# Kernel optimization log

Measured on AMD Instinct MI355X. Metric: run time of the kernel, lower is better.

Reference implementation:

```python
import jax, jax.numpy as jnp
import numpy as np

B, T, H, W = 4, 32, 160, 320
NF, FPF = 8, 8          # num_filters, features_per_filter
SPEED_DIM = 8           # speed_embedding output width
U = 64                  # internal LTC neurons (wiring units)
S = NF * FPF + SPEED_DIM  # 72 sensory inputs
M = 1                   # motor (output) neurons
ODE_UNFOLDS = 6
EPS = 1e-8


def setup_inputs() -> dict:
    key = jax.random.key(0)
    k = jax.random.split(key, 20)
    f32 = jnp.float32
    sp = (H // 8) * (W // 8)  # spatial size per filter after 3 stride-2 convs = 800
    d = {}
    d["input_sequence"] = jax.random.normal(k[0], (B, T, 3, H, W), f32)
    d["speed_sequence"] = jax.random.uniform(k[1], (B, T, 1), f32)
    # conv head params
    d["conv1_w"] = jax.random.normal(k[2], (16, 3, 5, 5), f32) * 0.05
    d["conv1_b"] = jnp.zeros((16,), f32)
    d["conv2_w"] = jax.random.normal(k[3], (32, 16, 5, 5), f32) * 0.05
    d["conv2_b"] = jnp.zeros((32,), f32)
    d["conv3_w"] = jax.random.normal(k[4], (NF, 32, 5, 5), f32) * 0.05
    d["conv3_b"] = jnp.zeros((NF,), f32)
    d["head_w"] = jax.random.normal(k[5], (NF, sp, FPF), f32) * 0.02  # per-filter Linear
    d["head_b"] = jnp.zeros((NF, FPF), f32)
    # speed embedding MLP (Dropout is identity at inference)
    d["se_w1"] = jax.random.normal(k[6], (1, 16), f32) * 0.5
    d["se_b1"] = jnp.zeros((16,), f32)
    d["se_w2"] = jax.random.normal(k[7], (16, SPEED_DIM), f32) * 0.3
    d["se_b2"] = jnp.zeros((SPEED_DIM,), f32)
    # LTC cell params (ncps-style init ranges)
    d["input_w"] = jnp.ones((S,), f32)
    d["input_b"] = jnp.zeros((S,), f32)
    d["gleak"] = jax.random.uniform(k[8], (U,), f32, 0.001, 1.0)
    d["vleak"] = jax.random.uniform(k[9], (U,), f32, -0.2, 0.2)
    d["cm"] = jax.random.uniform(k[10], (U,), f32, 0.4, 0.6)
    d["sigma"] = jax.random.uniform(k[11], (U, U), f32, 3.0, 8.0)
    d["mu"] = jax.random.uniform(k[12], (U, U), f32, 0.3, 0.8)
    d["w_syn"] = jax.random.uniform(k[13], (U, U), f32, 0.001, 1.0)
    d["erev"] = jnp.asarray(jax.random.bernoulli(k[14], 0.5, (U, U)), f32) * 2.0 - 1.0
    d["sensory_sigma"] = jax.random.uniform(k[15], (S, U), f32, 3.0, 8.0)
    d["sensory_mu"] = jax.random.uniform(k[16], (S, U), f32, 0.3, 0.8)
    d["sensory_w"] = jax.random.uniform(k[17], (S, U), f32, 0.001, 1.0)
    d["sensory_erev"] = jnp.asarray(jax.random.bernoulli(k[18], 0.5, (S, U)), f32) * 2.0 - 1.0
    d["output_w"] = jnp.ones((M,), f32)
    d["output_b"] = jnp.zeros((M,), f32)
    return d


def _conv(x, w, b, stride):
    y = jax.lax.conv_general_dilated(
        x, w, (stride, stride), [(2, 2), (2, 2)],
        dimension_numbers=("NCHW", "OIHW", "NCHW"))
    return jax.nn.relu(y + b[None, :, None, None])


def reference(input_sequence, speed_sequence, conv1_w, conv1_b, conv2_w, conv2_b,
              conv3_w, conv3_b, head_w, head_b, se_w1, se_b1, se_w2, se_b2,
              input_w, input_b, gleak, vleak, cm, sigma, mu, w_syn, erev,
              sensory_sigma, sensory_mu, sensory_w, sensory_erev, output_w, output_b):
    Bv, Tv = input_sequence.shape[:2]
    # ---- conv head over all frames at once ----
    x = input_sequence.reshape(Bv * Tv, 3, H, W)
    x = _conv(x, conv1_w, conv1_b, 2)
    x = _conv(x, conv2_w, conv2_b, 2)
    x = _conv(x, conv3_w, conv3_b, 2)          # [N, NF, H/8, W/8]
    x = x.reshape(Bv * Tv, NF, -1)             # [N, NF, 800]
    feats = jnp.einsum("nfp,fpk->nfk", x, head_w) + head_b  # per-filter Linear
    feats = feats.reshape(Bv, Tv, NF * FPF)    # [B, T, 64]
    # global-std normalization (torch .std() uses ddof=1)
    feats = feats / (jnp.std(feats, ddof=1) + 1e-5)
    # ---- speed embedding (vectorized over B,T) ----
    s = speed_sequence[..., :1]                # [B, T, 1]
    emb = jnp.tanh(jax.nn.relu(s @ se_w1 + se_b1) @ se_w2 + se_b2)  # [B, T, 8]
    xs = jnp.concatenate([feats, emb], axis=-1)   # [B, T, S]
    xs = jnp.swapaxes(xs, 0, 1)                   # [T, B, S]
    cm_t = cm * ODE_UNFOLDS  # cm / (elapsed_time / ode_unfolds), elapsed_time = 1.0

    def step(v, x_t):
        inp = x_t * input_w + input_b  # affine input mapping, [B, S]
        s_act = sensory_w * jax.nn.sigmoid((inp[:, :, None] - sensory_mu) * sensory_sigma)  # [B,S,U]
        w_num_s = jnp.sum(s_act * sensory_erev, axis=1)
        w_den_s = jnp.sum(s_act, axis=1)
        for _ in range(ODE_UNFOLDS):  # semi-implicit Euler unfolds
            w_act = w_syn * jax.nn.sigmoid((v[:, :, None] - mu) * sigma)  # [B,U,U]
            w_num = jnp.sum(w_act * erev, axis=1) + w_num_s
            w_den = jnp.sum(w_act, axis=1) + w_den_s
            v = (cm_t * v + gleak * vleak + w_num) / (cm_t + gleak + w_den + EPS)
        out = v[:, :M] * output_w + output_b  # affine output mapping on motor neurons
        return v, (out, v)

    v0 = jnp.zeros((Bv, U), feats.dtype)
    v_last, (outs, hs) = jax.lax.scan(step, v0, xs)
    readout = jnp.swapaxes(outs, 0, 1)  # [B, T, M]
    all_h = jnp.swapaxes(hs, 0, 1)      # [B, T, U]
    return readout, v_last, all_h
```

## Files before the change

### kernel.cpp

```cpp
#include <hip/hip_runtime.h>
#include <math.h>

#define BB 4
#define TT 32
#define NF 8
#define FPF 8
#define SDIM 8
#define UU 64
#define SS 72
#define UNFOLDS 6

typedef short short8 __attribute__((ext_vector_type(8)));
typedef float f32x4 __attribute__((ext_vector_type(4)));
union Frag { uint4 u; short8 s; };

__device__ __forceinline__ float fast_sigmoid(float x) {
    float e = exp2f(-1.44269504f * x);
    return __builtin_amdgcn_rcpf(1.0f + e);
}

__device__ __forceinline__ ushort f2b(float f) {
    union { float f; uint u; } a;
    a.f = f;
    uint u = a.u;
    return (ushort)((u + 0x7FFFu + ((u >> 16) & 1u)) >> 16);
}

__device__ __forceinline__ float bcast_lane(float v, int lane) {
    return __uint_as_float(__builtin_amdgcn_readlane(__float_as_uint(v), lane));
}

__device__ __forceinline__ void cvt_body(const float* __restrict__ in,
                                         ushort* __restrict__ outp, int idx) {
    int x = idx % 320;
    int r = idx / 320;
    int y = r % 160;
    int n = r / 160;
    const float* base = in + ((size_t)n * 3 * 160 + y) * 320 + x;
    float c0 = base[0];
    float c1 = base[160 * 320];
    float c2 = base[2 * 160 * 320];
    uint2 pk;
    pk.x = (uint)f2b(c0) | ((uint)f2b(c1) << 16);
    pk.y = (uint)f2b(c2);
    *(uint2*)(outp + ((size_t)((n * 164 + y + 2) * 328) + (x + 2)) * 4) = pk;
}

template <int HP, int WP, int H, int W, int CH>
__device__ __forceinline__ void halo_body(ushort* __restrict__ buf, int bid) {
    constexpr int TOPBOT = 2 * WP;
    constexpr int SIDE = WP - W;
    constexpr int NH = 2 * TOPBOT + H * SIDE;
    int idx = bid * 256 + threadIdx.x;
    if (idx >= 128 * NH) return;
    int n = idx / NH;
    int h = idx - n * NH;
    int y, x;
    if (h < TOPBOT) {
        y = h / WP;
        x = h % WP;
    } else if (h < 2 * TOPBOT) {
        int hh = h - TOPBOT;
        y = H + 2 + hh / WP;
        x = hh % WP;
    } else {
        int hh = h - 2 * TOPBOT;
        y = 2 + hh / SIDE;
        int xi = hh % SIDE;
        x = (xi < 2) ? xi : (W + xi);
    }
    ushort* p = buf + (((size_t)n * HP + y) * WP + x) * CH;
    if constexpr (CH == 4) {
        *(uint2*)p = make_uint2(0u, 0u);
    } else {
        uint4 z = make_uint4(0u, 0u, 0u, 0u);
#pragma unroll
        for (int i = 0; i < CH / 8; i++) *(uint4*)(p + i * 8) = z;
    }
}

__device__ __forceinline__ uint4 pack8(const ushort v[8]) {
    uint4 u;
    u.x = (uint)v[0] | ((uint)v[1] << 16);
    u.y = (uint)v[2] | ((uint)v[3] << 16);
    u.z = (uint)v[4] | ((uint)v[5] << 16);
    u.w = (uint)v[6] | ((uint)v[7] << 16);
    return u;
}

__device__ __forceinline__ void wswz1_body(const float* __restrict__ w, uint4* __restrict__ o,
                                           int i) {
    int lane = i & 63, s = i >> 6;
    int oc = lane & 15, q = lane >> 4;
    ushort v[8];
#pragma unroll
    for (int j = 0; j < 8; j++) {
        int k = q * 8 + j;
        int kx = k >> 2, c = k & 3;
        float f = (kx < 5 && c < 3) ? w[((oc * 3 + c) * 5 + s) * 5 + kx] : 0.f;
        v[j] = f2b(f);
    }
    o[i] = pack8(v);
}
__device__ __forceinline__ void wswz2_body(const float* __restrict__ w, uint4* __restrict__ o,
                                           int i) {
    int lane = i & 63;
    int ct = (i >> 6) & 1;
    int s = i >> 7;
    int ky = s / 3, kxp = s % 3;
    int oc = ct * 16 + (lane & 15);
    int q = lane >> 4, h = q >> 1;
    int kx = 2 * kxp + h;
    ushort v[8];
#pragma unroll
    for (int j = 0; j < 8; j++) {
        int ch = (q & 1) * 8 + j;
        float f = (kx < 5) ? w[((oc * 16 + ch) * 5 + ky) * 5 + kx] : 0.f;
        v[j] = f2b(f);
    }
    o[i] = pack8(v);
}
__device__ __forceinline__ void wswz3_body(const float* __restrict__ w, uint4* __restrict__ o,
                                           int i) {
    int lane = i & 63, s = i >> 6;
    int ky = s / 5, kx = s % 5;
    int oc = lane & 15, q = lane >> 4;
    ushort v[8];
#pragma unroll
    for (int j = 0; j < 8; j++) {
        int ch = q * 8 + j;
        float f = (oc < 8) ? w[((oc * 32 + ch) * 5 + ky) * 5 + kx] : 0.f;
        v[j] = f2b(f);
    }
    o[i] = pack8(v);
}

__global__ __launch_bounds__(256) void prep_kernel(
    const float* __restrict__ in_seq, ushort* __restrict__ inp1, ushort* __restrict__ c1out,
    ushort* __restrict__ c2out, const float* __restrict__ c1w, const float* __restrict__ c2w,
    const float* __restrict__ c3w, uint4* __restrict__ wz1, uint4* __restrict__ wz2,
    uint4* __restrict__ wz3) {
    int bid = blockIdx.x;
    if (bid < 25600) {
        cvt_body(in_seq, inp1, bid * 256 + threadIdx.x);
    } else if (bid < 25600 + 2032) {
        int hb = bid - 25600;
        if (hb < 1296)
            halo_body<164, 328, 160, 320, 4>(inp1, hb);
        else if (hb < 1296 + 488)
            halo_body<84, 164, 80, 160, 16>(c1out, hb - 1296);
        else
            halo_body<44, 84, 40, 80, 32>(c2out, hb - 1784);
    } else {
        int i = (bid - 27632) * 256 + threadIdx.x;
        if (i < 320)
            wswz1_body(c1w, wz1, i);
        else if (i < 2240)
            wswz2_body(c2w, wz2, i - 320);
        else
            wswz3_body(c3w, wz3, i - 2240);
    }
}

__global__ __launch_bounds__(256) void conv1_mfma(const ushort* __restrict__ inp,
                                                  const uint4* __restrict__ wswz,
                                                  const float* __restrict__ bias,
                                                  ushort* __restrict__ outp) {
    const int lane = threadIdx.x & 63;
    const int wid = threadIdx.x >> 6;
    const int col = lane & 15, q = lane >> 4;

    Frag A[5];
#pragma unroll
    for (int s = 0; s < 5; s++) A[s].u = wswz[s * 64 + lane];
    float b0 = bias[q * 4 + 0], b1 = bias[q * 4 + 1], b2 = bias[q * 4 + 2], b3 = bias[q * 4 + 3];

    int gw = blockIdx.x * 4 + wid;
#pragma unroll
    for (int t = 0; t < 4; t++) {
        int p0 = gw * 64 + t * 16;
        int n = p0 / 12800;
        int rem = p0 - n * 12800;
        int oy = rem / 160;
        int ox0 = rem - oy * 160;
        int ox = ox0 + col;
        uint e0 = ((uint)(n * 164 + oy * 2) * 328u + (uint)(ox * 2 + 2 * q)) * 4u;
        f32x4 acc = {0.f, 0.f, 0.f, 0.f};
#pragma unroll
        for (int s = 0; s < 5; s++) {
            Frag B;
            B.u = *(const uint4*)(inp + e0 + (uint)s * (328u * 4u));
            acc = __builtin_amdgcn_mfma_f32_16x16x32_bf16(A[s].s, B.s, acc, 0, 0, 0);
        }
        uint oe = ((uint)(n * 84 + oy + 2) * 164u + (uint)(ox + 2)) * 16u + q * 4u;
        uint2 pk;
        pk.x = (uint)f2b(fmaxf(acc[0] + b0, 0.f)) | ((uint)f2b(fmaxf(acc[1] + b1, 0.f)) << 16);
        pk.y = (uint)f2b(fmaxf(acc[2] + b2, 0.f)) | ((uint)f2b(fmaxf(acc[3] + b3, 0.f)) << 16);
        *(uint2*)(outp + oe) = pk;
    }
}

__global__ __launch_bounds__(256) void conv2_mfma(const ushort* __restrict__ inp,
                                                  const uint4* __restrict__ wswz,
                                                  const float* __restrict__ bias,
                                                  ushort* __restrict__ outp) {
    const int lane = threadIdx.x & 63;
    const int wid = threadIdx.x >> 6;
    const int col = lane & 15, q = lane >> 4;
    const int h = q >> 1, chh = q & 1;

    int gw = blockIdx.x * 4 + wid;
    uint eb[4];
#pragma unroll
    for (int t = 0; t < 4; t++) {
        int p0 = gw * 64 + t * 16;
        int n = p0 / 3200;
        int rem = p0 - n * 3200;
        int oy = rem / 80;
        int ox0 = rem - oy * 80;
        eb[t] = ((uint)(n * 84 + oy * 2) * 164u + (uint)((ox0 + col) * 2 + h)) * 16u + chh * 8u;
    }
    f32x4 acc[4][2];
#pragma unroll
    for (int t = 0; t < 4; t++) {
        acc[t][0] = {0.f, 0.f, 0.f, 0.f};
        acc[t][1] = {0.f, 0.f, 0.f, 0.f};
    }
#pragma unroll
    for (int s = 0; s < 15; s++) {
        const int ky = s / 3, kxp = s % 3;
        Frag A0, A1;
        A0.u = wswz[(s * 2 + 0) * 64 + lane];
        A1.u = wswz[(s * 2 + 1) * 64 + lane];
        const uint d = (uint)ky * (164u * 16u) + (uint)kxp * 32u;
#pragma unroll
        for (int t = 0; t < 4; t++) {
            Frag B;
            B.u = *(const uint4*)(inp + eb[t] + d);
            acc[t][0] = __builtin_amdgcn_mfma_f32_16x16x32_bf16(A0.s, B.s, acc[t][0], 0, 0, 0);
            acc[t][1] = __builtin_amdgcn_mfma_f32_16x16x32_bf16(A1.s, B.s, acc[t][1], 0, 0, 0);
        }
    }
    float ba[2][4];
#pragma unroll
    for (int c = 0; c < 2; c++)
#pragma unroll
        for (int r = 0; r < 4; r++) ba[c][r] = bias[c * 16 + q * 4 + r];
#pragma unroll
    for (int t = 0; t < 4; t++) {
        int p0 = gw * 64 + t * 16;
        int n = p0 / 3200;
        int rem = p0 - n * 3200;
        int oy = rem / 80;
        int ox0 = rem - oy * 80;
        int ox = ox0 + col;
        uint oe = ((uint)(n * 44 + oy + 2) * 84u + (uint)(ox + 2)) * 32u;
#pragma unroll
        for (int c = 0; c < 2; c++) {
            uint2 pk;
            pk.x = (uint)f2b(fmaxf(acc[t][c][0] + ba[c][0], 0.f)) |
                   ((uint)f2b(fmaxf(acc[t][c][1] + ba[c][1], 0.f)) << 16);
            pk.y = (uint)f2b(fmaxf(acc[t][c][2] + ba[c][2], 0.f)) |
                   ((uint)f2b(fmaxf(acc[t][c][3] + ba[c][3], 0.f)) << 16);
            *(uint2*)(outp + oe + (uint)c * 16u + (uint)q * 4u) = pk;
        }
    }
}

__global__ __launch_bounds__(256) void conv3_mfma(const ushort* __restrict__ inp,
                                                  const uint4* __restrict__ wswz,
                                                  const float* __restrict__ bias,
                                                  float* __restrict__ outp) {
    const int lane = threadIdx.x & 63;
    const int wid = threadIdx.x >> 6;
    const int col = lane & 15, q = lane >> 4;

    int gw = blockIdx.x * 4 + wid;
    uint eb[4];
#pragma unroll
    for (int t = 0; t < 4; t++) {
        int p0 = gw * 64 + t * 16;
        int n = p0 / 800;
        int pix = p0 - n * 800 + col;
        int oy = pix / 40;
        int ox = pix - oy * 40;
        eb[t] = ((uint)(n * 44 + oy * 2) * 84u + (uint)(ox * 2)) * 32u + q * 8u;
    }
    f32x4 acc[4];
#pragma unroll
    for (int t = 0; t < 4; t++) acc[t] = {0.f, 0.f, 0.f, 0.f};
#pragma unroll
    for (int s = 0; s < 25; s++) {
        const int ky = s / 5, kx = s % 5;
        Frag A;
        A.u = wswz[s * 64 + lane];
        const uint d = ((uint)ky * 84u + (uint)kx) * 32u;
#pragma unroll
        for (int t = 0; t < 4; t++) {
            Frag B;
            B.u = *(const uint4*)(inp + eb[t] + d);
            acc[t] = __builtin_amdgcn_mfma_f32_16x16x32_bf16(A.s, B.s, acc[t], 0, 0, 0);
        }
    }
    if (q < 2) {
        float b0 = bias[q * 4 + 0], b1 = bias[q * 4 + 1];
        float b2 = bias[q * 4 + 2], b3 = bias[q * 4 + 3];
#pragma unroll
        for (int t = 0; t < 4; t++) {
            int p0 = gw * 64 + t * 16;
            int n = p0 / 800;
            int p = p0 - n * 800 + col;
            float4 v;
            v.x = fmaxf(acc[t][0] + b0, 0.f);
            v.y = fmaxf(acc[t][1] + b1, 0.f);
            v.z = fmaxf(acc[t][2] + b2, 0.f);
            v.w = fmaxf(acc[t][3] + b3, 0.f);
            *(float4*)(outp + ((size_t)n * 800 + p) * 8 + q * 4) = v;
        }
    }
}

__global__ __launch_bounds__(256) void head_kernel(const float* __restrict__ x,
                                                   const float* __restrict__ hw,
                                                   const float* __restrict__ hb,
                                                   float* __restrict__ feats) {
    __shared__ float part[4][64];
    int n = blockIdx.x;
    int tid = threadIdx.x;
    int lane = tid & 63;
    int c = tid >> 6;
    int f = lane >> 3;
    int k = lane & 7;
    const float* xb = x + (size_t)n * 800 * 8 + f;
    const float* wb = hw + ((size_t)f * 800) * FPF + k;
    float acc = 0.0f;
    for (int p = c * 200; p < c * 200 + 200; p++)
        acc = fmaf(xb[(size_t)p * 8], wb[(size_t)p * FPF], acc);
    part[c][lane] = acc;
    __syncthreads();
    if (c == 0)
        feats[n * 64 + lane] = part[0][lane] + part[1][lane] + part[2][lane] + part[3][lane] +
                               hb[lane];
}

__global__ __launch_bounds__(256) void sensory256(
    const float* __restrict__ feats, const float* __restrict__ speed,
    const float* __restrict__ sew1, const float* __restrict__ seb1,
    const float* __restrict__ sew2, const float* __restrict__ seb2,
    const float* __restrict__ inw, const float* __restrict__ inb,
    const float* __restrict__ ssig, const float* __restrict__ smu,
    const float* __restrict__ sw, const float* __restrict__ serev,
    float* __restrict__ wns, float* __restrict__ wds) {
    __shared__ float2 red[256];
    __shared__ float2 part[4][64];
    int bid = blockIdx.x;
    int t = bid >> 2;
    int b = bid & 3;
    int tid = threadIdx.x;
    int u = tid & 63;
    int c = tid >> 6;
    int n = b * TT + t;

    float s = 0.0f, q = 0.0f;
    for (int i = tid; i < 8192; i += 256) {
        float x = feats[i];
        s += x;
        q += x * x;
    }
    red[tid] = make_float2(s, q);
    __syncthreads();
    for (int off = 128; off > 0; off >>= 1) {
        if (tid < off) {
            float2 o = red[tid + off];
            float2 m = red[tid];
            red[tid] = make_float2(m.x + o.x, m.y + o.y);
        }
        __syncthreads();
    }
    float mean = red[0].x / 8192.0f;
    float var = fmaxf((red[0].y - 8192.0f * mean * mean) / 8191.0f, 0.0f);
    float inv = 1.0f / (sqrtf(var) + 1e-5f);

    float sp = speed[n];
    float hh[16];
#pragma unroll
    for (int j = 0; j < 16; j++) hh[j] = fmaxf(fmaf(sp, sew1[j], seb1[j]), 0.0f);
    float embv[SDIM];
#pragma unroll
    for (int k = 0; k < SDIM; k++) {
        float a = seb2[k];
#pragma unroll
        for (int j = 0; j < 16; j++) a = fmaf(hh[j], sew2[j * SDIM + k], a);
        embv[k] = tanhf(a);
    }

    float num = 0.0f, den = 0.0f;
    int ss0 = c * 18;
#pragma unroll
    for (int i = 0; i < 18; i++) {
        int ss = ss0 + i;
        float xsv = (ss < 64) ? feats[n * 64 + ss] * inv : embv[ss - 64];
        float inp = fmaf(xsv, inw[ss], inb[ss]);
        int idx = ss * UU + u;
        float x = (inp - smu[idx]) * ssig[idx];
        float act = sw[idx] * fast_sigmoid(x);
        num = fmaf(act, serev[idx], num);
        den += act;
    }
    part[c][u] = make_float2(num, den);
    __syncthreads();
    if (c == 0) {
        float2 p0 = part[0][u], p1 = part[1][u], p2 = part[2][u], p3 = part[3][u];
        wns[bid * UU + u] = p0.x + p1.x + p2.x + p3.x;
        wds[bid * UU + u] = p0.y + p1.y + p2.y + p3.y;
    }
}

__global__ __launch_bounds__(512, 1) void scan_kernel(
    const float* __restrict__ wns, const float* __restrict__ wds,
    const float* __restrict__ gleak, const float* __restrict__ vleak,
    const float* __restrict__ cm, const float* __restrict__ sigma,
    const float* __restrict__ mu, const float* __restrict__ wsyn,
    const float* __restrict__ erev, const float* __restrict__ outw,
    const float* __restrict__ outb, float* __restrict__ dout) {
    int b = blockIdx.x;
    int tid = threadIdx.x;
    int u = tid & 63;
    int pc_s = __builtin_amdgcn_readfirstlane(tid >> 6);

    __shared__ float2 pbuf[2][8][64];

    float sA[8], sB[8], wer[8], w_[8];
#pragma unroll
    for (int i = 0; i < 8; i++) {
        int idx = (pc_s * 8 + i) * UU + u;
        float sg = sigma[idx];
        sA[i] = -1.44269504f * sg;
        sB[i] = -sA[i] * mu[idx];
        w_[i] = wsyn[idx];
        wer[i] = w_[i] * erev[idx];
    }
#pragma unroll
    for (int i = 0; i < 8; i++) {
        asm volatile("" : "+v"(sA[i]), "+v"(sB[i]), "+v"(wer[i]), "+v"(w_[i]));
    }
    float cmt = cm[u] * (float)UNFOLDS;
    float gl = gleak[u];
    float glvl = gl * vleak[u];
    float ow = outw[0], ob = outb[0];
    float v = 0.0f;
    int par = 0;

    float num_s = wns[(0 * BB + b) * UU + u];
    float den_s = wds[(0 * BB + b) * UU + u];
    for (int t = 0; t < TT; t++) {
        float nns = 0.f, nds = 0.f;
        if (t + 1 < TT) {
            nns = wns[((t + 1) * BB + b) * UU + u];
            nds = wds[((t + 1) * BB + b) * UU + u];
        }
#pragma unroll
        for (int k = 0; k < UNFOLDS; k++) {
            float num = 0.0f, den = 0.0f;
#pragma unroll
            for (int i = 0; i < 8; i++) {
                float vi = bcast_lane(v, pc_s * 8 + i);
                float e = exp2f(fmaf(vi, sA[i], sB[i]));
                float r = __builtin_amdgcn_rcpf(1.0f + e);
                num = fmaf(wer[i], r, num);
                den = fmaf(w_[i], r, den);
            }
            pbuf[par][pc_s][u] = make_float2(num, den);
            __builtin_amdgcn_sched_barrier(0);
            asm volatile("s_waitcnt lgkmcnt(0)" ::: "memory");
            __builtin_amdgcn_s_barrier();
            asm volatile("" ::: "memory");
            __builtin_amdgcn_sched_barrier(0);
            float nn = num_s, dd = den_s;
#pragma unroll
            for (int j = 0; j < 8; j++) {
                float2 p = pbuf[par][j][u];
                nn += p.x;
                dd += p.y;
            }
            float denom = cmt + gl + dd + 1e-8f;
            v = (fmaf(cmt, v, glvl) + nn) * __builtin_amdgcn_rcpf(denom);
            par ^= 1;
        }
        if (pc_s == 0) {
            dout[384 + (b * TT + t) * UU + u] = v;
            if (u == 0) dout[b * TT + t] = fmaf(v, ow, ob);
            if (t == TT - 1) dout[128 + b * UU + u] = v;
        }
        num_s = nns;
        den_s = nds;
    }
}

extern "C" void kernel_launch(void* const* d_in, const int* in_sizes, int n_in,
                              void* d_out, int out_size, void* d_ws, size_t ws_size,
                              hipStream_t stream) {
    const float* in_seq = (const float*)d_in[0];
    const float* speed = (const float*)d_in[1];
    const float* c1w = (const float*)d_in[2];
    const float* c1b = (const float*)d_in[3];
    const float* c2w = (const float*)d_in[4];
    const float* c2b = (const float*)d_in[5];
    const float* c3w = (const float*)d_in[6];
    const float* c3b = (const float*)d_in[7];
    const float* hw = (const float*)d_in[8];
    const float* hb = (const float*)d_in[9];
    const float* sew1 = (const float*)d_in[10];
    const float* seb1 = (const float*)d_in[11];
    const float* sew2 = (const float*)d_in[12];
    const float* seb2 = (const float*)d_in[13];
    const float* inw = (const float*)d_in[14];
    const float* inb = (const float*)d_in[15];
    const float* gleak = (const float*)d_in[16];
    const float* vleak = (const float*)d_in[17];
    const float* cm = (const float*)d_in[18];
    const float* sigma = (const float*)d_in[19];
    const float* mu = (const float*)d_in[20];
    const float* wsyn = (const float*)d_in[21];
    const float* erev = (const float*)d_in[22];
    const float* ssig = (const float*)d_in[23];
    const float* smu = (const float*)d_in[24];
    const float* sw = (const float*)d_in[25];
    const float* serev = (const float*)d_in[26];
    const float* outw = (const float*)d_in[27];
    const float* outb = (const float*)d_in[28];

    char* ws = (char*)d_ws;
    float* out = (float*)d_out;

    size_t off = 0;
    auto alloc = [&](size_t bytes) {
        size_t o = off;
        off += (bytes + 255) & ~(size_t)255;
        return o;
    };
    ushort* inp1 = (ushort*)(ws + alloc((size_t)128 * 164 * 328 * 4 * 2));
    ushort* c1out = (ushort*)(ws + alloc((size_t)128 * 84 * 164 * 16 * 2));
    ushort* c2out = (ushort*)(ws + alloc((size_t)128 * 44 * 84 * 32 * 2));
    float* c3out = (float*)(ws + alloc((size_t)128 * 800 * 8 * 4));
    float* feats = (float*)(ws + alloc(8192 * 4));
    float* wns = (float*)(ws + alloc(8192 * 4));
    float* wds = (float*)(ws + alloc(8192 * 4));
    uint4* wz1 = (uint4*)(ws + alloc(5 * 64 * 16));
    uint4* wz2 = (uint4*)(ws + alloc(30 * 64 * 16));
    uint4* wz3 = (uint4*)(ws + alloc(25 * 64 * 16));

    prep_kernel<<<27647, 256, 0, stream>>>(in_seq, inp1, c1out, c2out, c1w, c2w, c3w, wz1,
                                           wz2, wz3);

    conv1_mfma<<<6400, 256, 0, stream>>>(inp1, wz1, c1b, c1out);
    conv2_mfma<<<1600, 256, 0, stream>>>(c1out, wz2, c2b, c2out);
    conv3_mfma<<<400, 256, 0, stream>>>(c2out, wz3, c3b, c3out);

    head_kernel<<<128, 256, 0, stream>>>(c3out, hw, hb, feats);

    sensory256<<<128, 256, 0, stream>>>(feats, speed, sew1, seb1, sew2, seb2, inw, inb,
                                        ssig, smu, sw, serev, wns, wds);

    scan_kernel<<<BB, 512, 0, stream>>>(wns, wds, gleak, vleak, cm, sigma, mu, wsyn, erev,
                                        outw, outb, out);
}
```

Before: 257.0 us.

## Run LTC scan in a single wavefront per batch, dropping LDS reduction and barriers

After: 525.4 us. 104% more time.

```diff
diff --git a/kernel.cpp b/kernel.cpp
--- a/kernel.cpp
+++ b/kernel.cpp
@@ -416,7 +416,7 @@
     }
 }
 
-__global__ __launch_bounds__(512, 1) void scan_kernel(
+__global__ __launch_bounds__(64, 1) void scan_kernel(
     const float* __restrict__ wns, const float* __restrict__ wds,
     const float* __restrict__ gleak, const float* __restrict__ vleak,
     const float* __restrict__ cm, const float* __restrict__ sigma,
@@ -424,16 +424,12 @@
     const float* __restrict__ erev, const float* __restrict__ outw,
     const float* __restrict__ outb, float* __restrict__ dout) {
     int b = blockIdx.x;
-    int tid = threadIdx.x;
-    int u = tid & 63;
-    int pc_s = __builtin_amdgcn_readfirstlane(tid >> 6);
-
-    __shared__ float2 pbuf[2][8][64];
-
-    float sA[8], sB[8], wer[8], w_[8];
-#pragma unroll
-    for (int i = 0; i < 8; i++) {
-        int idx = (pc_s * 8 + i) * UU + u;
+    int u = threadIdx.x;
+
+    float sA[64], sB[64], wer[64], w_[64];
+#pragma unroll
+    for (int i = 0; i < 64; i++) {
+        int idx = i * UU + u;
         float sg = sigma[idx];
         sA[i] = -1.44269504f * sg;
         sB[i] = -sA[i] * mu[idx];
@@ -441,7 +437,7 @@
         wer[i] = w_[i] * erev[idx];
     }
 #pragma unroll
-    for (int i = 0; i < 8; i++) {
+    for (int i = 0; i < 64; i++) {
         asm volatile("" : "+v"(sA[i]), "+v"(sB[i]), "+v"(wer[i]), "+v"(w_[i]));
     }
     float cmt = cm[u] * (float)UNFOLDS;
@@ -449,7 +445,6 @@
     float glvl = gl * vleak[u];
     float ow = outw[0], ob = outb[0];
     float v = 0.0f;
-    int par = 0;
 
     float num_s = wns[(0 * BB + b) * UU + u];
     float den_s = wds[(0 * BB + b) * UU + u];
@@ -461,37 +456,21 @@
         }
 #pragma unroll
         for (int k = 0; k < UNFOLDS; k++) {
-            float num = 0.0f, den = 0.0f;
-#pragma unroll
-            for (int i = 0; i < 8; i++) {
-                float vi = bcast_lane(v, pc_s * 8 + i);
+            float num = num_s, den = den_s;
+#pragma unroll
+            for (int i = 0; i < 64; i++) {
+                float vi = bcast_lane(v, i);
                 float e = exp2f(fmaf(vi, sA[i], sB[i]));
                 float r = __builtin_amdgcn_rcpf(1.0f + e);
                 num = fmaf(wer[i], r, num);
                 den = fmaf(w_[i], r, den);
             }
-            pbuf[par][pc_s][u] = make_float2(num, den);
-            __builtin_amdgcn_sched_barrier(0);
-            asm volatile("s_waitcnt lgkmcnt(0)" ::: "memory");
-            __builtin_amdgcn_s_barrier();
-            asm volatile("" ::: "memory");
-            __builtin_amdgcn_sched_barrier(0);
-            float nn = num_s, dd = den_s;
-#pragma unroll
-            for (int j = 0; j < 8; j++) {
-                float2 p = pbuf[par][j][u];
-                nn += p.x;
-                dd += p.y;
-            }
-            float denom = cmt + gl + dd + 1e-8f;
-            v = (fmaf(cmt, v, glvl) + nn) * __builtin_amdgcn_rcpf(denom);
-            par ^= 1;
-        }
-        if (pc_s == 0) {
-            dout[384 + (b * TT + t) * UU + u] = v;
-            if (u == 0) dout[b * TT + t] = fmaf(v, ow, ob);
-            if (t == TT - 1) dout[128 + b * UU + u] = v;
-        }
+            float denom = cmt + gl + den + 1e-8f;
+            v = (fmaf(cmt, v, glvl) + num) * __builtin_amdgcn_rcpf(denom);
+        }
+        dout[384 + (b * TT + t) * UU + u] = v;
+        if (u == 0) dout[b * TT + t] = fmaf(v, ow, ob);
+        if (t == TT - 1) dout[128 + b * UU + u] = v;
         num_s = nns;
         den_s = nds;
     }
@@ -562,6 +541,6 @@
     sensory256<<<128, 256, 0, stream>>>(feats, speed, sew1, seb1, sew2, seb2, inw, inb,
                                         ssig, smu, sw, serev, wns, wds);
 
-    scan_kernel<<<BB, 512, 0, stream>>>(wns, wds, gleak, vleak, cm, sigma, mu, wsyn, erev,
-                                        outw, outb, out);
-}
+    scan_kernel<<<BB, 64, 0, stream>>>(wns, wds, gleak, vleak, cm, sigma, mu, wsyn, erev,
+                                       outw, outb, out);
+}
```
